# Optimization experiments

Measured on AMD Instinct MI355X. Metric: run time of the kernel, lower is better.

The kernel has to match this reference:

```python
import jax, jax.numpy as jnp
import numpy as np

# Static config mirroring init_kwargs
RADIUS = 0.7
K = 32            # nsamples
SPATIAL_STRIDE = 32
TKS = 3           # temporal_kernel_size
TSTRIDE = 2       # temporal_stride
DIM = 512


def fps(xyz, m):
    # Furthest point sampling (pointnet2 semantics: start at index 0).
    # xyz: [N,3] -> [m] int32 indices
    N = xyz.shape[0]
    def body(carry, _):
        mind, last = carry
        d = jnp.sum((xyz - xyz[last]) ** 2, axis=-1)
        mind = jnp.minimum(mind, d)
        nxt = jnp.argmax(mind).astype(jnp.int32)
        return (mind, nxt), nxt
    init = (jnp.full((N,), 1e10, xyz.dtype), jnp.int32(0))
    _, rest = jax.lax.scan(body, init, None, length=m - 1)
    return jnp.concatenate([jnp.zeros((1,), jnp.int32), rest])


def ball_query(nb, anchors, r, k):
    # pointnet2 ball_query: first-k in-radius neighbors in original order,
    # padded with the first found index (0 if none within radius).
    # nb: [..., N, 3], anchors: [..., M, 3] -> [..., M, k] int32
    N = nb.shape[-2]
    d2 = jnp.sum((anchors[..., :, None, :] - nb[..., None, :, :]) ** 2, axis=-1)  # [...,M,N]
    ar = jnp.arange(N, dtype=jnp.int32)
    cand = jnp.where(d2 < r * r, ar, N)
    cand = jnp.sort(cand, axis=-1)[..., :k]
    first = cand[..., :1]
    first = jnp.where(first == N, 0, first)
    return jnp.where(cand == N, first, cand)


def setup_inputs() -> dict:
    key = jax.random.key(0)
    k1, k2, k3, k4, k5 = jax.random.split(key, 5)
    B, T, N = 2, 15, 2048
    inp = {
        "input": jax.random.normal(k1, (B, T, N, 3), dtype=jnp.float32),
        "W_d": jax.random.normal(k2, (DIM, 4), dtype=jnp.float32) * 0.5,   # conv_d 1x1, no bias
        "W_f": jax.random.normal(k3, (DIM, 1), dtype=jnp.float32) * 0.5,   # conv_f 1x1, no bias
        "W_pos": jax.random.normal(k4, (DIM, 4), dtype=jnp.float32) * 0.5, # pos_embedding conv1d k=1
        "b_pos": jax.random.normal(k5, (DIM,), dtype=jnp.float32) * 0.1,
    }
    return inp


def reference(input, W_d, W_f, W_pos, b_pos):
    B, T, N, _ = input.shape
    xyz = input[..., :3]
    feat = input[..., 2:3]                      # z channel as feature [B,T,N,1]
    # replicate temporal padding [1,1]
    xyz_p = jnp.concatenate([xyz[:, :1], xyz, xyz[:, -1:]], axis=1)    # [B,T+2,N,3]
    feat_p = jnp.concatenate([feat[:, :1], feat, feat[:, -1:]], axis=1)
    tr = (TKS - 1) // 2
    Tp = T + 2
    anchor_t = np.arange(tr, Tp - tr, TSTRIDE)  # static output-frame indices
    To = len(anchor_t)
    M = N // SPATIAL_STRIDE

    anchor_frames = xyz_p[:, anchor_t]          # [B,To,N,3]
    fps_idx = jax.vmap(jax.vmap(lambda p: fps(p, M)))(anchor_frames)   # [B,To,M]
    anchor_xyz = jnp.take_along_axis(anchor_frames, fps_idx[..., None], axis=2)  # [B,To,M,3]

    pooled = None
    for dt in range(-tr, tr + 1):               # temporal kernel taps (static, size 3)
        nb = xyz_p[:, anchor_t + dt]            # [B,To,N,3]
        idx = ball_query(nb, anchor_xyz, RADIUS, K)                    # [B,To,M,K]
        flat = idx.reshape(B, To, M * K, 1)
        gx = jnp.take_along_axis(nb, flat, axis=2).reshape(B, To, M, K, 3)
        disp = gx - anchor_xyz[:, :, :, None, :]                       # xyz displacement
        td = jnp.full((B, To, M, K, 1), float(dt), input.dtype)        # t displacement (i - t)
        d4 = jnp.concatenate([disp, td], axis=-1)                      # [B,To,M,K,4]
        d_out = jnp.einsum('btmkf,df->btmkd', d4, W_d)
        nf = feat_p[:, anchor_t + dt]                                  # [B,To,N,1]
        gf = jnp.take_along_axis(nf, flat, axis=2).reshape(B, To, M, K, 1)
        f_out = jnp.einsum('btmkc,dc->btmkd', gf, W_f)
        feature = jnp.max(f_out + d_out, axis=3)                       # spatial max-pool -> [B,To,M,DIM]
        pooled = feature if pooled is None else jnp.maximum(pooled, feature)  # temporal max-pool

    # Encoder glue: append frame time (t_out+1), 1x1 conv pos-embed, add, relu
    tvals = (jnp.arange(To, dtype=input.dtype) + 1.0)[None, :, None, None]
    tcol = jnp.broadcast_to(tvals, (B, To, M, 1))
    xyzt = jnp.concatenate([anchor_xyz, tcol], axis=-1).reshape(B, To * M, 4)
    feats = pooled.reshape(B, To * M, DIM)
    pos = jnp.einsum('bnf,df->bnd', xyzt, W_pos) + b_pos
    return jax.nn.relu(pos + feats)
```

## Files before the change

### kernel.cpp

```cpp
#include <hip/hip_runtime.h>
#include <hip/hip_bf16.h>

#define BB 2
#define TT 15
#define NN 2048
#define TO 8
#define MM 64
#define KH 32
#define DIMD 512
#define R2 0.49f

typedef float v2f __attribute__((ext_vector_type(2)));
typedef unsigned long long ull;

template<int CTRL>
__device__ __forceinline__ unsigned dppu(unsigned x) {
    return (unsigned)__builtin_amdgcn_update_dpp((int)x, (int)x, CTRL, 0xF, 0xF, false);
}

__global__ __launch_bounds__(256) void fps_kernel(const float* __restrict__ input,
                                                  float* __restrict__ anchor_xyz) {
#pragma clang fp contract(off)
    __shared__ float sxyz[NN * 3];
    __shared__ ull   sK[2][4];
    __shared__ float wout[MM * 3];
    int blk = blockIdx.x;
    int b = blk >> 3, f = blk & 7;
    const float* src = input + ((size_t)(b * TT + 2 * f)) * NN * 3;
    int tid = threadIdx.x, w = tid >> 6;

    const float4* s4 = (const float4*)(src + tid * 24);
    float4 v0 = s4[0], v1 = s4[1], v2 = s4[2], v3 = s4[3], v4 = s4[4], v5 = s4[5];
    float4* l4 = (float4*)(sxyz + tid * 24);
    l4[0] = v0; l4[1] = v1; l4[2] = v2; l4[3] = v3; l4[4] = v4; l4[5] = v5;

    v2f PX[4], PY[4], PZ[4], MD[4];
    PX[0] = (v2f){v0.x, v0.w}; PY[0] = (v2f){v0.y, v1.x}; PZ[0] = (v2f){v0.z, v1.y};
    PX[1] = (v2f){v1.z, v2.y}; PY[1] = (v2f){v1.w, v2.z}; PZ[1] = (v2f){v2.x, v2.w};
    PX[2] = (v2f){v3.x, v3.w}; PY[2] = (v2f){v3.y, v4.x}; PZ[2] = (v2f){v3.z, v4.y};
    PX[3] = (v2f){v4.z, v5.y}; PY[3] = (v2f){v4.w, v5.z}; PZ[3] = (v2f){v5.x, v5.w};
#pragma unroll
    for (int p = 0; p < 4; ++p) MD[p] = (v2f){1e10f, 1e10f};
    unsigned base = (unsigned)(NN - tid * 8);

    float lx = src[0], ly = src[1], lz = src[2];
    if (tid == 0) { wout[0] = lx; wout[1] = ly; wout[2] = lz; }

    for (int it = 1; it < MM; ++it) {
        int pp = it & 1;
        v2f L0 = (v2f){lx, lx}, L1 = (v2f){ly, ly}, L2 = (v2f){lz, lz};
#pragma unroll
        for (int p = 0; p < 4; ++p) {
            v2f dx = PX[p] - L0, dy = PY[p] - L1, dz = PZ[p] - L2;
            v2f u1 = dx * dx, u2 = dy * dy, u3 = dz * dz;
            v2f d = (u1 + u2) + u3;
            MD[p] = __builtin_elementwise_min(MD[p], d);
        }
        ull k[8];
#pragma unroll
        for (int p = 0; p < 4; ++p) {
            k[2 * p]     = (((ull)__float_as_uint(MD[p].x)) << 32) | (ull)(base - 2 * p);
            k[2 * p + 1] = (((ull)__float_as_uint(MD[p].y)) << 32) | (ull)(base - 2 * p - 1);
        }
#pragma unroll
        for (int st = 1; st < 8; st <<= 1)
#pragma unroll
            for (int j = 0; j < 8; j += 2 * st)
                if (k[j + st] > k[j]) k[j] = k[j + st];
        unsigned khi = (unsigned)(k[0] >> 32), klo = (unsigned)k[0];

#define DPP_STEP(CTRL) { \
            unsigned ohi = dppu<CTRL>(khi), olo = dppu<CTRL>(klo); \
            ull ok = (((ull)ohi) << 32) | olo, ck = (((ull)khi) << 32) | klo; \
            if (ok > ck) { khi = ohi; klo = olo; } }
        DPP_STEP(0xB1)
        DPP_STEP(0x4E)
        DPP_STEP(0x141)
        DPP_STEP(0x140)
        DPP_STEP(0x142)
        DPP_STEP(0x143)
#undef DPP_STEP
        if ((tid & 63) == 63) sK[pp][w] = (((ull)khi) << 32) | klo;
        __syncthreads();
        ull k0 = sK[pp][0], k1 = sK[pp][1], k2 = sK[pp][2], k3 = sK[pp][3];
        if (k1 > k0) k0 = k1;
        if (k3 > k2) k2 = k3;
        if (k2 > k0) k0 = k2;
        unsigned widx = NN - (unsigned)k0;
        lx = sxyz[3 * widx]; ly = sxyz[3 * widx + 1]; lz = sxyz[3 * widx + 2];
        if (tid == 0) { wout[it * 3 + 0] = lx; wout[it * 3 + 1] = ly; wout[it * 3 + 2] = lz; }
    }

    __syncthreads();
    float* out = anchor_xyz + (size_t)blk * MM * 3;
    if (tid < MM * 3) out[tid] = wout[tid];
}

__global__ __launch_bounds__(256) void encode_kernel(const float* __restrict__ input,
                                                     const float* __restrict__ W_d,
                                                     const float* __restrict__ W_f,
                                                     const float* __restrict__ W_pos,
                                                     const float* __restrict__ b_pos,
                                                     const float* __restrict__ anchor_xyz,
                                                     float* __restrict__ outp) {
    __shared__ float hx[2][KH], hy[2][KH], hz[2][KH];
    __shared__ int swtot[2][4];
    int bid = blockIdx.x;
    int b = bid >> 9;
    int rem = bid & 511;
    int f = rem >> 6;
    int m = rem & 63;
    int tid = threadIdx.x, lane = tid & 63, w = tid >> 6;

    const float* anc = anchor_xyz + (size_t)(((b << 3) + f) * MM + m) * 3;
    float ax = anc[0], ay = anc[1], az = anc[2];

    int d0 = tid, d1 = tid + 256;
    float4 wd0 = ((const float4*)W_d)[d0];
    float4 wd1 = ((const float4*)W_d)[d1];
    float  wf0 = W_f[d0], wf1 = W_f[d1];
    float p0 = -INFINITY, p1 = -INFINITY;

    for (int dt = -1; dt <= 1; ++dt) {
        int pp = (dt + 1) & 1;
        int frame = 2 * f + dt;
        frame = frame < 0 ? 0 : (frame > 14 ? 14 : frame);
        const float* src = input + ((size_t)(b * TT + frame)) * NN * 3;

        float px[8], py[8], pz[8];
        const float4* s4 = (const float4*)(src + tid * 24);
        float4 v0 = s4[0], v1 = s4[1], v2 = s4[2], v3 = s4[3], v4 = s4[4], v5 = s4[5];
        px[0] = v0.x; py[0] = v0.y; pz[0] = v0.z;
        px[1] = v0.w; py[1] = v1.x; pz[1] = v1.y;
        px[2] = v1.z; py[2] = v1.w; pz[2] = v2.x;
        px[3] = v2.y; py[3] = v2.z; pz[3] = v2.w;
        px[4] = v3.x; py[4] = v3.y; pz[4] = v3.z;
        px[5] = v3.w; py[5] = v4.x; pz[5] = v4.y;
        px[6] = v4.z; py[6] = v4.w; pz[6] = v5.x;
        px[7] = v5.y; py[7] = v5.z; pz[7] = v5.w;

        unsigned hit = 0; int cnt = 0;
#pragma unroll
        for (int j = 0; j < 8; ++j) {
            float dx = ax - px[j], dy = ay - py[j], dz = az - pz[j];
            float d2 = __fadd_rn(__fadd_rn(__fmul_rn(dx, dx), __fmul_rn(dy, dy)),
                                 __fmul_rn(dz, dz));
            if (d2 < R2) { hit |= 1u << j; cnt++; }
        }
        int s = cnt;
#pragma unroll
        for (int off = 1; off < 64; off <<= 1) {
            int o = __shfl_up(s, off);
            if (lane >= off) s += o;
        }
        if (lane == 63) swtot[pp][w] = s;
        __syncthreads();
        int wavebase = 0, total = 0;
#pragma unroll
        for (int ww = 0; ww < 4; ++ww) {
            int t2 = swtot[pp][ww];
            total += t2;
            if (ww < w) wavebase += t2;
        }
        int r = wavebase + s - cnt;
#pragma unroll
        for (int j = 0; j < 8; ++j) {
            if (hit & (1u << j)) {
                if (r < KH) { hx[pp][r] = px[j]; hy[pp][r] = py[j]; hz[pp][r] = pz[j]; }
                r++;
            }
        }
        if (total == 0 && tid == 0) { hx[pp][0] = px[0]; hy[pp][0] = py[0]; hz[pp][0] = pz[0]; }
        __syncthreads();

        int nh = (total == 0) ? 1 : (total < KH ? total : KH);
        float dtf = (float)dt;
        float q0 = -INFINITY, q1 = -INFINITY;
        int k = 0;
        for (; k + 2 <= nh; k += 2) {
            float gx0 = hx[pp][k],     gy0 = hy[pp][k],     gz0 = hz[pp][k];
            float gx1 = hx[pp][k + 1], gy1 = hy[pp][k + 1], gz1 = hz[pp][k + 1];
            float dx0 = gx0 - ax, dy0 = gy0 - ay, dz0 = gz0 - az;
            float dx1 = gx1 - ax, dy1 = gy1 - ay, dz1 = gz1 - az;
            float u0 = dx0 * wd0.x + dy0 * wd0.y + dz0 * wd0.z + dtf * wd0.w + gz0 * wf0;
            float u1 = dx0 * wd1.x + dy0 * wd1.y + dz0 * wd1.z + dtf * wd1.w + gz0 * wf1;
            float t0 = dx1 * wd0.x + dy1 * wd0.y + dz1 * wd0.z + dtf * wd0.w + gz1 * wf0;
            float t1 = dx1 * wd1.x + dy1 * wd1.y + dz1 * wd1.z + dtf * wd1.w + gz1 * wf1;
            p0 = fmaxf(p0, u0); p1 = fmaxf(p1, u1);
            q0 = fmaxf(q0, t0); q1 = fmaxf(q1, t1);
        }
        if (k < nh) {
            float gx0 = hx[pp][k], gy0 = hy[pp][k], gz0 = hz[pp][k];
            float dx0 = gx0 - ax, dy0 = gy0 - ay, dz0 = gz0 - az;
            float u0 = dx0 * wd0.x + dy0 * wd0.y + dz0 * wd0.z + dtf * wd0.w + gz0 * wf0;
            float u1 = dx0 * wd1.x + dy0 * wd1.y + dz0 * wd1.z + dtf * wd1.w + gz0 * wf1;
            p0 = fmaxf(p0, u0); p1 = fmaxf(p1, u1);
        }
        p0 = fmaxf(p0, q0); p1 = fmaxf(p1, q1);
    }

    float4 wp0 = ((const float4*)W_pos)[d0];
    float4 wp1 = ((const float4*)W_pos)[d1];
    float tv = (float)(f + 1);
    float pos0 = ax * wp0.x + ay * wp0.y + az * wp0.z + tv * wp0.w + b_pos[d0];
    float pos1 = ax * wp1.x + ay * wp1.y + az * wp1.z + tv * wp1.w + b_pos[d1];
    float o0 = fmaxf(pos0 + p0, 0.0f);
    float o1 = fmaxf(pos1 + p1, 0.0f);
    size_t row = ((size_t)b * (TO * MM) + f * MM + m) * DIMD;
    outp[row + d0] = o0;
    outp[row + d1] = o1;
}

extern "C" void kernel_launch(void* const* d_in, const int* in_sizes, int n_in,
                              void* d_out, int out_size, void* d_ws, size_t ws_size,
                              hipStream_t stream) {
    const float* input = (const float*)d_in[0];
    const float* W_d   = (const float*)d_in[1];
    const float* W_f   = (const float*)d_in[2];
    const float* W_pos = (const float*)d_in[3];
    const float* b_pos = (const float*)d_in[4];
    float* anchor = (float*)d_ws;

    fps_kernel<<<16, 256, 0, stream>>>(input, anchor);
    encode_kernel<<<1024, 256, 0, stream>>>(input, W_d, W_f, W_pos, b_pos, anchor,
                                            (float*)d_out);
}
```

Baseline: 50.02 us.

## Carry winner coords through FPS reduction, prefetch frames and pack-math in encoder

The FPS kernel stops staging all points in LDS and carries each candidate's coordinates alongside its key through the reduction. The winning wave publishes them directly, which removes the dependent LDS gather on every iteration. The encoder prefetches all three temporal frames up front and replaces the shfl-based scan with a DPP inclusive scan. It also stores hits as float4 and evaluates the two output channels with packed v2f FMA. The cost is more registers and extra selects in the FPS reduction, and the packed FMA may round differently from the original expression order.

```diff
diff --git a/kernel.cpp b/kernel.cpp
--- a/kernel.cpp
+++ b/kernel.cpp
@@ -18,12 +18,23 @@
     return (unsigned)__builtin_amdgcn_update_dpp((int)x, (int)x, CTRL, 0xF, 0xF, false);
 }
 
+__device__ __forceinline__ int wave_incl_scan(int x) {
+    int s = x;
+    s += __builtin_amdgcn_update_dpp(0, s, 0x111, 0xF, 0xF, true);
+    s += __builtin_amdgcn_update_dpp(0, s, 0x112, 0xF, 0xF, true);
+    s += __builtin_amdgcn_update_dpp(0, s, 0x114, 0xF, 0xF, true);
+    s += __builtin_amdgcn_update_dpp(0, s, 0x118, 0xF, 0xF, true);
+    s += __builtin_amdgcn_update_dpp(0, s, 0x142, 0xA, 0xF, false);
+    s += __builtin_amdgcn_update_dpp(0, s, 0x143, 0xC, 0xF, false);
+    return s;
+}
+
 __global__ __launch_bounds__(256) void fps_kernel(const float* __restrict__ input,
                                                   float* __restrict__ anchor_xyz) {
 #pragma clang fp contract(off)
-    __shared__ float sxyz[NN * 3];
-    __shared__ ull   sK[2][4];
-    __shared__ float wout[MM * 3];
+    __shared__ float4 sA[2][4];
+    __shared__ float  sB[2][4];
+    __shared__ float  wout[MM * 3];
     int blk = blockIdx.x;
     int b = blk >> 3, f = blk & 7;
     const float* src = input + ((size_t)(b * TT + 2 * f)) * NN * 3;
@@ -31,8 +42,6 @@
 
     const float4* s4 = (const float4*)(src + tid * 24);
     float4 v0 = s4[0], v1 = s4[1], v2 = s4[2], v3 = s4[3], v4 = s4[4], v5 = s4[5];
-    float4* l4 = (float4*)(sxyz + tid * 24);
-    l4[0] = v0; l4[1] = v1; l4[2] = v2; l4[3] = v3; l4[4] = v4; l4[5] = v5;
 
     v2f PX[4], PY[4], PZ[4], MD[4];
     PX[0] = (v2f){v0.x, v0.w}; PY[0] = (v2f){v0.y, v1.x}; PZ[0] = (v2f){v0.z, v1.y};
@@ -56,18 +65,23 @@
             v2f d = (u1 + u2) + u3;
             MD[p] = __builtin_elementwise_min(MD[p], d);
         }
-        ull k[8];
+        ull k[8]; float cx[8], cy[8], cz[8];
 #pragma unroll
         for (int p = 0; p < 4; ++p) {
             k[2 * p]     = (((ull)__float_as_uint(MD[p].x)) << 32) | (ull)(base - 2 * p);
             k[2 * p + 1] = (((ull)__float_as_uint(MD[p].y)) << 32) | (ull)(base - 2 * p - 1);
+            cx[2 * p] = PX[p].x; cy[2 * p] = PY[p].x; cz[2 * p] = PZ[p].x;
+            cx[2 * p + 1] = PX[p].y; cy[2 * p + 1] = PY[p].y; cz[2 * p + 1] = PZ[p].y;
         }
 #pragma unroll
         for (int st = 1; st < 8; st <<= 1)
 #pragma unroll
             for (int j = 0; j < 8; j += 2 * st)
-                if (k[j + st] > k[j]) k[j] = k[j + st];
-        unsigned khi = (unsigned)(k[0] >> 32), klo = (unsigned)k[0];
+                if (k[j + st] > k[j]) {
+                    k[j] = k[j + st]; cx[j] = cx[j + st]; cy[j] = cy[j + st]; cz[j] = cz[j + st];
+                }
+        ull myk = k[0];
+        unsigned khi = (unsigned)(myk >> 32), klo = (unsigned)myk;
 
 #define DPP_STEP(CTRL) { \
             unsigned ohi = dppu<CTRL>(khi), olo = dppu<CTRL>(klo); \
@@ -80,14 +94,24 @@
         DPP_STEP(0x142)
         DPP_STEP(0x143)
 #undef DPP_STEP
-        if ((tid & 63) == 63) sK[pp][w] = (((ull)khi) << 32) | klo;
+        ull wmax = (((ull)(unsigned)__builtin_amdgcn_readlane((int)khi, 63)) << 32)
+                 |  (ull)(unsigned)__builtin_amdgcn_readlane((int)klo, 63);
+        if (myk == wmax) {
+            sA[pp][w] = make_float4(__uint_as_float((unsigned)(wmax >> 32)),
+                                    __uint_as_float((unsigned)wmax), cx[0], cy[0]);
+            sB[pp][w] = cz[0];
+        }
         __syncthreads();
-        ull k0 = sK[pp][0], k1 = sK[pp][1], k2 = sK[pp][2], k3 = sK[pp][3];
-        if (k1 > k0) k0 = k1;
-        if (k3 > k2) k2 = k3;
-        if (k2 > k0) k0 = k2;
-        unsigned widx = NN - (unsigned)k0;
-        lx = sxyz[3 * widx]; ly = sxyz[3 * widx + 1]; lz = sxyz[3 * widx + 2];
+        float4 a0 = sA[pp][0], a1 = sA[pp][1], a2 = sA[pp][2], a3 = sA[pp][3];
+        float b0 = sB[pp][0], b1 = sB[pp][1], b2 = sB[pp][2], b3 = sB[pp][3];
+        ull q0 = (((ull)__float_as_uint(a0.x)) << 32) | __float_as_uint(a0.y);
+        ull q1 = (((ull)__float_as_uint(a1.x)) << 32) | __float_as_uint(a1.y);
+        ull q2 = (((ull)__float_as_uint(a2.x)) << 32) | __float_as_uint(a2.y);
+        ull q3 = (((ull)__float_as_uint(a3.x)) << 32) | __float_as_uint(a3.y);
+        if (q1 > q0) { q0 = q1; a0.z = a1.z; a0.w = a1.w; b0 = b1; }
+        if (q3 > q2) { q2 = q3; a2.z = a3.z; a2.w = a3.w; b2 = b3; }
+        if (q2 > q0) { q0 = q2; a0.z = a2.z; a0.w = a2.w; b0 = b2; }
+        lx = a0.z; ly = a0.w; lz = b0;
         if (tid == 0) { wout[it * 3 + 0] = lx; wout[it * 3 + 1] = ly; wout[it * 3 + 2] = lz; }
     }
 
@@ -103,7 +127,7 @@
                                                      const float* __restrict__ b_pos,
                                                      const float* __restrict__ anchor_xyz,
                                                      float* __restrict__ outp) {
-    __shared__ float hx[2][KH], hy[2][KH], hz[2][KH];
+    __shared__ float4 hxyz[2][KH];
     __shared__ int swtot[2][4];
     int bid = blockIdx.x;
     int b = bid >> 9;
@@ -119,17 +143,26 @@
     float4 wd0 = ((const float4*)W_d)[d0];
     float4 wd1 = ((const float4*)W_d)[d1];
     float  wf0 = W_f[d0], wf1 = W_f[d1];
-    float p0 = -INFINITY, p1 = -INFINITY;
-
-    for (int dt = -1; dt <= 1; ++dt) {
-        int pp = (dt + 1) & 1;
-        int frame = 2 * f + dt;
+    v2f WX = (v2f){wd0.x, wd1.x}, WY = (v2f){wd0.y, wd1.y};
+    v2f WZ = (v2f){wd0.z, wd1.z}, WW = (v2f){wd0.w, wd1.w};
+    v2f WF = (v2f){wf0, wf1};
+    v2f P = (v2f){-INFINITY, -INFINITY}, Q = (v2f){-INFINITY, -INFINITY};
+
+    float4 V[3][6];
+#pragma unroll
+    for (int q = 0; q < 3; ++q) {
+        int frame = 2 * f + q - 1;
         frame = frame < 0 ? 0 : (frame > 14 ? 14 : frame);
-        const float* src = input + ((size_t)(b * TT + frame)) * NN * 3;
-
+        const float4* s4 = (const float4*)(input + ((size_t)(b * TT + frame)) * NN * 3 + tid * 24);
+#pragma unroll
+        for (int i = 0; i < 6; ++i) V[q][i] = s4[i];
+    }
+
+#pragma unroll
+    for (int q = 0; q < 3; ++q) {
+        int pp = q & 1;
+        float4 v0 = V[q][0], v1 = V[q][1], v2 = V[q][2], v3 = V[q][3], v4 = V[q][4], v5 = V[q][5];
         float px[8], py[8], pz[8];
-        const float4* s4 = (const float4*)(src + tid * 24);
-        float4 v0 = s4[0], v1 = s4[1], v2 = s4[2], v3 = s4[3], v4 = s4[4], v5 = s4[5];
         px[0] = v0.x; py[0] = v0.y; pz[0] = v0.z;
         px[1] = v0.w; py[1] = v1.x; pz[1] = v1.y;
         px[2] = v1.z; py[2] = v1.w; pz[2] = v2.x;
@@ -147,12 +180,7 @@
                                  __fmul_rn(dz, dz));
             if (d2 < R2) { hit |= 1u << j; cnt++; }
         }
-        int s = cnt;
-#pragma unroll
-        for (int off = 1; off < 64; off <<= 1) {
-            int o = __shfl_up(s, off);
-            if (lane >= off) s += o;
-        }
+        int s = wave_incl_scan(cnt);
         if (lane == 63) swtot[pp][w] = s;
         __syncthreads();
         int wavebase = 0, total = 0;
@@ -166,46 +194,46 @@
 #pragma unroll
         for (int j = 0; j < 8; ++j) {
             if (hit & (1u << j)) {
-                if (r < KH) { hx[pp][r] = px[j]; hy[pp][r] = py[j]; hz[pp][r] = pz[j]; }
+                if (r < KH) hxyz[pp][r] = make_float4(px[j], py[j], pz[j], 0.f);
                 r++;
             }
         }
-        if (total == 0 && tid == 0) { hx[pp][0] = px[0]; hy[pp][0] = py[0]; hz[pp][0] = pz[0]; }
+        if (total == 0 && tid == 0) hxyz[pp][0] = make_float4(px[0], py[0], pz[0], 0.f);
         __syncthreads();
 
         int nh = (total == 0) ? 1 : (total < KH ? total : KH);
-        float dtf = (float)dt;
-        float q0 = -INFINITY, q1 = -INFINITY;
+        float dtf = (float)(q - 1);
+        v2f DTW = (v2f){dtf, dtf} * WW;
         int k = 0;
         for (; k + 2 <= nh; k += 2) {
-            float gx0 = hx[pp][k],     gy0 = hy[pp][k],     gz0 = hz[pp][k];
-            float gx1 = hx[pp][k + 1], gy1 = hy[pp][k + 1], gz1 = hz[pp][k + 1];
-            float dx0 = gx0 - ax, dy0 = gy0 - ay, dz0 = gz0 - az;
-            float dx1 = gx1 - ax, dy1 = gy1 - ay, dz1 = gz1 - az;
-            float u0 = dx0 * wd0.x + dy0 * wd0.y + dz0 * wd0.z + dtf * wd0.w + gz0 * wf0;
-            float u1 = dx0 * wd1.x + dy0 * wd1.y + dz0 * wd1.z + dtf * wd1.w + gz0 * wf1;
-            float t0 = dx1 * wd0.x + dy1 * wd0.y + dz1 * wd0.z + dtf * wd0.w + gz1 * wf0;
-            float t1 = dx1 * wd1.x + dy1 * wd1.y + dz1 * wd1.z + dtf * wd1.w + gz1 * wf1;
-            p0 = fmaxf(p0, u0); p1 = fmaxf(p1, u1);
-            q0 = fmaxf(q0, t0); q1 = fmaxf(q1, t1);
+            float4 g0 = hxyz[pp][k], g1 = hxyz[pp][k + 1];
+            v2f u0 = DTW, u1 = DTW;
+            u0 += (v2f){g0.z, g0.z} * WF;            u1 += (v2f){g1.z, g1.z} * WF;
+            u0 += (v2f){g0.x - ax, g0.x - ax} * WX;  u1 += (v2f){g1.x - ax, g1.x - ax} * WX;
+            u0 += (v2f){g0.y - ay, g0.y - ay} * WY;  u1 += (v2f){g1.y - ay, g1.y - ay} * WY;
+            u0 += (v2f){g0.z - az, g0.z - az} * WZ;  u1 += (v2f){g1.z - az, g1.z - az} * WZ;
+            P = __builtin_elementwise_max(P, u0);
+            Q = __builtin_elementwise_max(Q, u1);
         }
         if (k < nh) {
-            float gx0 = hx[pp][k], gy0 = hy[pp][k], gz0 = hz[pp][k];
-            float dx0 = gx0 - ax, dy0 = gy0 - ay, dz0 = gz0 - az;
-            float u0 = dx0 * wd0.x + dy0 * wd0.y + dz0 * wd0.z + dtf * wd0.w + gz0 * wf0;
-            float u1 = dx0 * wd1.x + dy0 * wd1.y + dz0 * wd1.z + dtf * wd1.w + gz0 * wf1;
-            p0 = fmaxf(p0, u0); p1 = fmaxf(p1, u1);
-        }
-        p0 = fmaxf(p0, q0); p1 = fmaxf(p1, q1);
+            float4 g0 = hxyz[pp][k];
+            v2f u0 = DTW;
+            u0 += (v2f){g0.z, g0.z} * WF;
+            u0 += (v2f){g0.x - ax, g0.x - ax} * WX;
+            u0 += (v2f){g0.y - ay, g0.y - ay} * WY;
+            u0 += (v2f){g0.z - az, g0.z - az} * WZ;
+            P = __builtin_elementwise_max(P, u0);
+        }
     }
+    P = __builtin_elementwise_max(P, Q);
 
     float4 wp0 = ((const float4*)W_pos)[d0];
     float4 wp1 = ((const float4*)W_pos)[d1];
     float tv = (float)(f + 1);
     float pos0 = ax * wp0.x + ay * wp0.y + az * wp0.z + tv * wp0.w + b_pos[d0];
     float pos1 = ax * wp1.x + ay * wp1.y + az * wp1.z + tv * wp1.w + b_pos[d1];
-    float o0 = fmaxf(pos0 + p0, 0.0f);
-    float o1 = fmaxf(pos1 + p1, 0.0f);
+    float o0 = fmaxf(pos0 + P.x, 0.0f);
+    float o1 = fmaxf(pos1 + P.y, 0.0f);
     size_t row = ((size_t)b * (TO * MM) + f * MM + m) * DIMD;
     outp[row + d0] = o0;
     outp[row + d1] = o1;
```

Measured after the change: 85.15 us. 1.7x slower.
